# Kernel optimization log

Hardware: AMD Instinct MI355X
Metric: run time of the kernel (lower is better)

The kernel has to match this reference:

```python
import jax, jax.numpy as jnp
import numpy as np

NUM_HEADS = 16


def setup_inputs() -> dict:
    key = jax.random.key(0)
    k1, k2, k3, k4 = jax.random.split(key, 4)
    B, S, D = 2, 2048, 1024
    x = jax.random.normal(k1, (B, S, D), dtype=jnp.float32)
    W_qkv = jax.random.normal(k2, (D, 3 * D), dtype=jnp.float32) * (1.0 / np.sqrt(D))
    b_qkv = jax.random.normal(k3, (3 * D,), dtype=jnp.float32) * 0.02
    W_out = jax.random.normal(k4, (D, D), dtype=jnp.float32) * (1.0 / np.sqrt(D))
    return {"x": x, "W_qkv": W_qkv, "b_qkv": b_qkv, "W_out": W_out}


def reference(x, W_qkv, b_qkv, W_out):
    B, S, D = x.shape
    H = NUM_HEADS
    Hd = D // H
    scale = 1.0 / np.sqrt(Hd)

    qkv = x @ W_qkv + b_qkv                      # [B, S, 3D]
    q, k, v = jnp.split(qkv, 3, axis=-1)
    # [B, H, S, Hd]
    q = q.reshape(B, S, H, Hd).transpose(0, 2, 1, 3)
    k = k.reshape(B, S, H, Hd).transpose(0, 2, 1, 3)
    v = v.reshape(B, S, H, Hd).transpose(0, 2, 1, 3)

    scores = jnp.einsum('bhqd,bhkd->bhqk', q, k) * scale  # [B, H, S, S]
    causal = jnp.triu(jnp.full((S, S), -jnp.inf, dtype=scores.dtype), k=1)
    scores = scores + causal
    attn = jax.nn.softmax(scores.astype(jnp.float32), axis=-1).astype(q.dtype)

    ctx = jnp.einsum('bhqk,bhkd->bhqd', attn, v)           # [B, H, S, Hd]
    ctx = ctx.transpose(0, 2, 1, 3).reshape(B, S, D)
    return ctx @ W_out
```

## Files before the change

### kernel.cpp

```cpp
#include <hip/hip_runtime.h>
#include <hip/hip_bf16.h>

typedef __bf16 bf16x8 __attribute__((ext_vector_type(8)));
typedef float f32x4 __attribute__((ext_vector_type(4)));

typedef __attribute__((address_space(1))) void gv_t;
typedef __attribute__((address_space(3))) void lv_t;

__device__ __forceinline__ unsigned short f2bf(float f) {
    unsigned int u = __float_as_uint(f);
    unsigned int r = (u + 0x7fffu + ((u >> 16) & 1u)) >> 16;
    return (unsigned short)r;
}

__device__ __forceinline__ unsigned int cvt_pk_bf16(float a, float b) {
    unsigned int r;
    asm("v_cvt_pk_bf16_f32 %0, %1, %2" : "=v"(r) : "v"(a), "v"(b));
    return r;
}

__global__ void convert_f32_bf16(const float* __restrict__ in,
                                 unsigned short* __restrict__ out, int n4) {
    int i = blockIdx.x * blockDim.x + threadIdx.x;
    if (i >= n4) return;
    float4 v = reinterpret_cast<const float4*>(in)[i];
    ushort4 o;
    o.x = f2bf(v.x); o.y = f2bf(v.y); o.z = f2bf(v.z); o.w = f2bf(v.w);
    reinterpret_cast<ushort4*>(out)[i] = o;
}

__global__ void transpose_convert(const float* __restrict__ in,
                                  unsigned short* __restrict__ out,
                                  int K, int N) {
    __shared__ float t[32][33];
    int n0 = blockIdx.x * 32, k0 = blockIdx.y * 32;
    t[threadIdx.y][threadIdx.x] = in[(size_t)(k0 + threadIdx.y) * N + (n0 + threadIdx.x)];
    __syncthreads();
    out[(size_t)(n0 + threadIdx.y) * K + (k0 + threadIdx.x)] = f2bf(t[threadIdx.x][threadIdx.y]);
}

template <bool BIAS, bool OUT_BF16, bool QSCALE>
__global__ __launch_bounds__(256) void gemm_bt(const unsigned short* __restrict__ A,
                                               const unsigned short* __restrict__ Bt,
                                               const float* __restrict__ bias,
                                               void* __restrict__ Cv,
                                               int M, int N, int K) {
    __shared__ alignas(16) unsigned short As[128 * 32];
    __shared__ alignas(16) unsigned short Bs[128 * 32];

    const int t = threadIdx.x;
    const int lane = t & 63;
    const int wid = t >> 6;
    const int wr = wid >> 1, wc = wid & 1;
    const int m0 = blockIdx.y * 128, n0 = blockIdx.x * 128;

    f32x4 acc[4][4] = {};

    for (int k0 = 0; k0 < K; k0 += 32) {
#pragma unroll
        for (int i = 0; i < 2; ++i) {
            int c = i * 256 + t;
            int row = c >> 2;
            int col = (c & 3) * 8;
            const unsigned short* ga = A + (size_t)(m0 + row) * K + k0 + col;
            const unsigned short* gb = Bt + (size_t)(n0 + row) * K + k0 + col;
            __builtin_amdgcn_global_load_lds((gv_t*)ga, (lv_t*)(As + c * 8), 16, 0, 0);
            __builtin_amdgcn_global_load_lds((gv_t*)gb, (lv_t*)(Bs + c * 8), 16, 0, 0);
        }
        __syncthreads();

        bf16x8 af[4], bfr[4];
#pragma unroll
        for (int i = 0; i < 4; ++i)
            af[i] = *reinterpret_cast<const bf16x8*>(As + (wr * 64 + i * 16 + (lane & 15)) * 32 + (lane >> 4) * 8);
#pragma unroll
        for (int j = 0; j < 4; ++j)
            bfr[j] = *reinterpret_cast<const bf16x8*>(Bs + (wc * 64 + j * 16 + (lane & 15)) * 32 + (lane >> 4) * 8);
#pragma unroll
        for (int i = 0; i < 4; ++i)
#pragma unroll
            for (int j = 0; j < 4; ++j)
                acc[i][j] = __builtin_amdgcn_mfma_f32_16x16x32_bf16(af[i], bfr[j], acc[i][j], 0, 0, 0);
        __syncthreads();
    }

#pragma unroll
    for (int i = 0; i < 4; ++i) {
        int row = m0 + wr * 64 + i * 16 + (lane >> 4) * 4;
#pragma unroll
        for (int j = 0; j < 4; ++j) {
            int col = n0 + wc * 64 + j * 16 + (lane & 15);
            float bv = 0.0f;
            if (BIAS) bv = bias[col];
#pragma unroll
            for (int r = 0; r < 4; ++r) {
                float v = acc[i][j][r] + bv;
                if constexpr (QSCALE) { if (col < 1024) v *= 0.125f; }
                if constexpr (OUT_BF16)
                    ((unsigned short*)Cv)[(size_t)(row + r) * N + col] = f2bf(v);
                else
                    ((float*)Cv)[(size_t)(row + r) * N + col] = v;
            }
        }
    }
}

__global__ __launch_bounds__(512) void attn_fwd(const unsigned short* __restrict__ qkv,
                                                unsigned short* __restrict__ ctx,
                                                int S) {
    const int TD = 3072, D = 1024;
    __shared__ alignas(16) unsigned short Ks[2][64 * 64];
    __shared__ alignas(16) unsigned short Vt[2][64 * 64];
    __shared__ alignas(16) unsigned short Ps[8][16 * 64];

    const int t = threadIdx.x, lane = t & 63;
    const int w_all = t >> 6;
    const int w_loc = w_all & 3;
    const bool is_hi = (w_all < 4);
    const int l15 = lane & 15, l4 = lane >> 4;
    const int pid = blockIdx.x;
    const int bh = blockIdx.y;
    const int b = bh >> 4, h = bh & 15;
    const int QT_lo = pid, QT_hi = 31 - pid;
    const int QT = is_hi ? QT_hi : QT_lo;

    const size_t base = ((size_t)b * S) * TD + (size_t)h * 64;
    const unsigned short* qp = qkv + base;
    const unsigned short* kp = qkv + base + D;
    const unsigned short* vp = qkv + base + 2 * D;

    bf16x8 aq[2];
    {
        const unsigned short* g = qp + (size_t)(QT * 64 + w_loc * 16 + l15) * TD + l4 * 8;
        aq[0] = *reinterpret_cast<const bf16x8*>(g);
        aq[1] = *reinterpret_cast<const bf16x8*>(g + 32);
    }

    f32x4 oc[4] = {};
    float mR = -1e30f, lR = 0.f;
    const float L2E = 1.44269504f;

    auto stageK = [&](int j0, int buf) {
        int c = t;
        int row = c >> 3, hh = c & 7;
        const unsigned short* src = kp + (size_t)(j0 * 64 + row) * TD + ((hh ^ (row & 7)) * 8);
        __builtin_amdgcn_global_load_lds((gv_t*)src, (lv_t*)(Ks[buf] + c * 8), 16, 0, 0);
    };
    const int v_hd = (t & 31) * 2, v_kvb = (t >> 5) * 4;
    unsigned int vv[4];
    auto loadV = [&](int j0) {
        const unsigned short* vsrc = vp + (size_t)(j0 * 64 + v_kvb) * TD + v_hd;
#pragma unroll
        for (int e = 0; e < 4; ++e)
            vv[e] = *reinterpret_cast<const unsigned int*>(vsrc + (size_t)e * TD);
    };
    auto writeV = [&](int buf) {
        unsigned int r0a = __builtin_amdgcn_perm(vv[1], vv[0], 0x05040100u);
        unsigned int r0b = __builtin_amdgcn_perm(vv[3], vv[2], 0x05040100u);
        unsigned int r1a = __builtin_amdgcn_perm(vv[1], vv[0], 0x07060302u);
        unsigned int r1b = __builtin_amdgcn_perm(vv[3], vv[2], 0x07060302u);
        int g0 = (v_kvb >> 3) ^ (v_hd & 7);
        int g1 = (v_kvb >> 3) ^ ((v_hd + 1) & 7);
        int sub = v_kvb & 7;
        *reinterpret_cast<uint2*>(Vt[buf] + v_hd * 64 + g0 * 8 + sub) = make_uint2(r0a, r0b);
        *reinterpret_cast<uint2*>(Vt[buf] + (v_hd + 1) * 64 + g1 * 8 + sub) = make_uint2(r1a, r1b);
    };

    auto compute = [&](bool diag, int buf) {
        f32x4 sc[4];
        __builtin_amdgcn_s_setprio(1);
#pragma unroll
        for (int jn = 0; jn < 4; ++jn) {
            f32x4 s = {};
#pragma unroll
            for (int kk = 0; kk < 2; ++kk) {
                int row = jn * 16 + l15;
                int g = (kk * 4 + l4) ^ (l15 & 7);
                bf16x8 ak = *reinterpret_cast<const bf16x8*>(Ks[buf] + row * 64 + g * 8);
                s = __builtin_amdgcn_mfma_f32_16x16x32_bf16(ak, aq[kk], s, 0, 0, 0);
            }
            sc[jn] = s;
        }
        __builtin_amdgcn_s_setprio(0);
        if (diag) {
            int ql = w_loc * 16 + l15;
#pragma unroll
            for (int jn = 0; jn < 4; ++jn)
#pragma unroll
                for (int r = 0; r < 4; ++r)
                    if (jn * 16 + l4 * 4 + r > ql) sc[jn][r] = -1e30f;
        }
        float pm = -1e30f;
#pragma unroll
        for (int jn = 0; jn < 4; ++jn)
            pm = fmaxf(fmaxf(pm, fmaxf(sc[jn][0], sc[jn][1])),
                       fmaxf(sc[jn][2], sc[jn][3]));
        pm = fmaxf(pm, __shfl_xor(pm, 16));
        pm = fmaxf(pm, __shfl_xor(pm, 32));
        if (__any(pm > mR + 8.0f)) {
            float mnew = fmaxf(mR, pm);
            float alpha = exp2f((mR - mnew) * L2E);
            mR = mnew;
            lR *= alpha;
#pragma unroll
            for (int jc = 0; jc < 4; ++jc) oc[jc] *= alpha;
        }
        float mn2 = mR * L2E;
        float ps = 0.f;
#pragma unroll
        for (int jn = 0; jn < 4; ++jn) {
            float p0 = exp2f(sc[jn][0] * L2E - mn2);
            float p1 = exp2f(sc[jn][1] * L2E - mn2);
            float p2 = exp2f(sc[jn][2] * L2E - mn2);
            float p3 = exp2f(sc[jn][3] * L2E - mn2);
            sc[jn][0] = p0; sc[jn][1] = p1; sc[jn][2] = p2; sc[jn][3] = p3;
            ps += (p0 + p1) + (p2 + p3);
        }
        ps += __shfl_xor(ps, 16);
        ps += __shfl_xor(ps, 32);
        lR += ps;
        const int q = l15;
#pragma unroll
        for (int jn = 0; jn < 4; ++jn) {
            unsigned int lo = cvt_pk_bf16(sc[jn][0], sc[jn][1]);
            unsigned int hi = cvt_pk_bf16(sc[jn][2], sc[jn][3]);
            int kv0 = jn * 16 + l4 * 4;
            int g = (kv0 >> 3) ^ (q & 7);
            *reinterpret_cast<uint2*>(Ps[w_all] + q * 64 + g * 8 + (kv0 & 7)) = make_uint2(lo, hi);
        }
        __builtin_amdgcn_s_setprio(1);
#pragma unroll
        for (int kk = 0; kk < 2; ++kk) {
            int gq = (kk * 4 + l4) ^ (q & 7);
            bf16x8 bp = *reinterpret_cast<const bf16x8*>(Ps[w_all] + q * 64 + gq * 8);
#pragma unroll
            for (int jc = 0; jc < 4; ++jc) {
                int hdrow = jc * 16 + l15;
                int gv = (kk * 4 + l4) ^ (l15 & 7);
                bf16x8 av = *reinterpret_cast<const bf16x8*>(Vt[buf] + hdrow * 64 + gv * 8);
                oc[jc] = __builtin_amdgcn_mfma_f32_16x16x32_bf16(av, bp, oc[jc], 0, 0, 0);
            }
        }
        __builtin_amdgcn_s_setprio(0);
    };

    stageK(0, 0);
    loadV(0);
    writeV(0);
    __syncthreads();

    for (int j0 = 0; j0 <= QT_hi; ++j0) {
        const int cur = j0 & 1, nxt = cur ^ 1;
        const bool have_next = (j0 < QT_hi);
        if (have_next) {
            stageK(j0 + 1, nxt);
            loadV(j0 + 1);
        }
        if (j0 <= QT) compute(j0 == QT, cur);
        if (have_next) writeV(nxt);
        __syncthreads();
    }

    {
        float inv = 1.0f / lR;
        size_t qg = (size_t)QT * 64 + w_loc * 16 + l15;
        unsigned short* crow = ctx + ((size_t)b * S + qg) * D + h * 64;
#pragma unroll
        for (int jc = 0; jc < 4; ++jc) {
            unsigned int pk0 = cvt_pk_bf16(oc[jc][0] * inv, oc[jc][1] * inv);
            unsigned int pk1 = cvt_pk_bf16(oc[jc][2] * inv, oc[jc][3] * inv);
            *reinterpret_cast<uint2*>(crow + jc * 16 + l4 * 4) = make_uint2(pk0, pk1);
        }
    }
}

extern "C" void kernel_launch(void* const* d_in, const int* in_sizes, int n_in,
                              void* d_out, int out_size, void* d_ws, size_t ws_size,
                              hipStream_t stream) {
    const float* x = (const float*)d_in[0];
    const float* Wqkv = (const float*)d_in[1];
    const float* bqkv = (const float*)d_in[2];
    const float* Wout = (const float*)d_in[3];
    float* out = (float*)d_out;

    const int B = 2, S = 2048, D = 1024, TD = 3072;
    const int M = B * S;

    char* ws = (char*)d_ws;
    unsigned short* x_bf  = (unsigned short*)(ws);
    unsigned short* wqkvT = (unsigned short*)(ws + 8388608);
    unsigned short* woutT = (unsigned short*)(ws + 14680064);
    unsigned short* qkv   = (unsigned short*)(ws + 16777216);
    unsigned short* ctx   = (unsigned short*)(ws + 41943040);

    convert_f32_bf16<<<dim3((M * D / 4 + 255) / 256), dim3(256), 0, stream>>>(x, x_bf, M * D / 4);
    transpose_convert<<<dim3(TD / 32, D / 32), dim3(32, 32), 0, stream>>>(Wqkv, wqkvT, D, TD);
    transpose_convert<<<dim3(D / 32, D / 32), dim3(32, 32), 0, stream>>>(Wout, woutT, D, D);

    gemm_bt<true, true, true><<<dim3(TD / 128, M / 128), dim3(256), 0, stream>>>(
        x_bf, wqkvT, bqkv, (void*)qkv, M, TD, D);

    attn_fwd<<<dim3(16, 32), dim3(512), 0, stream>>>(qkv, ctx, S);

    gemm_bt<false, false, false><<<dim3(D / 128, M / 128), dim3(256), 0, stream>>>(
        ctx, woutT, nullptr, (void*)out, M, D, D);
}
```

Baseline: 139.8 us.

## Double GEMM K-tile to 64 and add XCD-aware block swizzling

The GEMM K-step grows from 32 to 64, halving the number of loop iterations and barriers per output tile and doubling LDS staging. Both the GEMM and the attention kernel remap the linear block index so that consecutive blocks, which the hardware spreads across the 8 XCDs, instead land in contiguous groups that share L2-resident operands. The larger LDS tiles use a 128-byte row stride with no padding or swizzle, which may raise LDS bank conflicts on the fragment reads. The GEMM remap assumes the block count is divisible by 8, and the attention remap hardcodes a 16x32 grid.

```diff
diff --git a/kernel.cpp b/kernel.cpp
--- a/kernel.cpp
+++ b/kernel.cpp
@@ -45,23 +45,29 @@
                                                const float* __restrict__ bias,
                                                void* __restrict__ Cv,
                                                int M, int N, int K) {
-    __shared__ alignas(16) unsigned short As[128 * 32];
-    __shared__ alignas(16) unsigned short Bs[128 * 32];
+    __shared__ alignas(16) unsigned short As[128 * 64];
+    __shared__ alignas(16) unsigned short Bs[128 * 64];
 
     const int t = threadIdx.x;
     const int lane = t & 63;
     const int wid = t >> 6;
     const int wr = wid >> 1, wc = wid & 1;
-    const int m0 = blockIdx.y * 128, n0 = blockIdx.x * 128;
+    const int l15 = lane & 15, l4 = lane >> 4;
+
+    const int nwg = gridDim.x * gridDim.y;
+    const int lin = blockIdx.y * gridDim.x + blockIdx.x;
+    const int cpx = nwg >> 3;
+    const int swz = (lin & 7) * cpx + (lin >> 3);
+    const int m0 = (swz / gridDim.x) * 128, n0 = (swz % gridDim.x) * 128;
 
     f32x4 acc[4][4] = {};
 
-    for (int k0 = 0; k0 < K; k0 += 32) {
-#pragma unroll
-        for (int i = 0; i < 2; ++i) {
+    for (int k0 = 0; k0 < K; k0 += 64) {
+#pragma unroll
+        for (int i = 0; i < 4; ++i) {
             int c = i * 256 + t;
-            int row = c >> 2;
-            int col = (c & 3) * 8;
+            int row = c >> 3;
+            int col = (c & 7) * 8;
             const unsigned short* ga = A + (size_t)(m0 + row) * K + k0 + col;
             const unsigned short* gb = Bt + (size_t)(n0 + row) * K + k0 + col;
             __builtin_amdgcn_global_load_lds((gv_t*)ga, (lv_t*)(As + c * 8), 16, 0, 0);
@@ -69,27 +75,33 @@
         }
         __syncthreads();
 
-        bf16x8 af[4], bfr[4];
+        bf16x8 af[4][2], bfr[4][2];
 #pragma unroll
         for (int i = 0; i < 4; ++i)
-            af[i] = *reinterpret_cast<const bf16x8*>(As + (wr * 64 + i * 16 + (lane & 15)) * 32 + (lane >> 4) * 8);
+#pragma unroll
+            for (int kk = 0; kk < 2; ++kk)
+                af[i][kk] = *reinterpret_cast<const bf16x8*>(As + (wr * 64 + i * 16 + l15) * 64 + kk * 32 + l4 * 8);
 #pragma unroll
         for (int j = 0; j < 4; ++j)
-            bfr[j] = *reinterpret_cast<const bf16x8*>(Bs + (wc * 64 + j * 16 + (lane & 15)) * 32 + (lane >> 4) * 8);
-#pragma unroll
-        for (int i = 0; i < 4; ++i)
-#pragma unroll
-            for (int j = 0; j < 4; ++j)
-                acc[i][j] = __builtin_amdgcn_mfma_f32_16x16x32_bf16(af[i], bfr[j], acc[i][j], 0, 0, 0);
+#pragma unroll
+            for (int kk = 0; kk < 2; ++kk)
+                bfr[j][kk] = *reinterpret_cast<const bf16x8*>(Bs + (wc * 64 + j * 16 + l15) * 64 + kk * 32 + l4 * 8);
+#pragma unroll
+        for (int kk = 0; kk < 2; ++kk)
+#pragma unroll
+            for (int i = 0; i < 4; ++i)
+#pragma unroll
+                for (int j = 0; j < 4; ++j)
+                    acc[i][j] = __builtin_amdgcn_mfma_f32_16x16x32_bf16(af[i][kk], bfr[j][kk], acc[i][j], 0, 0, 0);
         __syncthreads();
     }
 
 #pragma unroll
     for (int i = 0; i < 4; ++i) {
-        int row = m0 + wr * 64 + i * 16 + (lane >> 4) * 4;
+        int row = m0 + wr * 64 + i * 16 + l4 * 4;
 #pragma unroll
         for (int j = 0; j < 4; ++j) {
-            int col = n0 + wc * 64 + j * 16 + (lane & 15);
+            int col = n0 + wc * 64 + j * 16 + l15;
             float bv = 0.0f;
             if (BIAS) bv = bias[col];
 #pragma unroll
@@ -118,8 +130,10 @@
     const int w_loc = w_all & 3;
     const bool is_hi = (w_all < 4);
     const int l15 = lane & 15, l4 = lane >> 4;
-    const int pid = blockIdx.x;
-    const int bh = blockIdx.y;
+    const int lin = blockIdx.y * 16 + blockIdx.x;
+    const int swz = (lin & 7) * 64 + (lin >> 3);
+    const int pid = swz & 15;
+    const int bh = swz >> 4;
     const int b = bh >> 4, h = bh & 15;
     const int QT_lo = pid, QT_hi = 31 - pid;
     const int QT = is_hi ? QT_hi : QT_lo;
```

Measured after the change: 152.8 us. +9.2%, slower.
